# Kernel tuning notes

Measured on AMD Instinct MI355X. Metric: run time of the kernel, lower is better.

## Reference

```python
import jax, jax.numpy as jnp
import numpy as np

N_NODES = 100000
N_EDGES = 1600000
IN_DIM, H1, H2, OUT_DIM = 128, 64, 64, 64


def _glorot(key, shape):
    fan_in, fan_out = shape
    lim = np.sqrt(6.0 / (fan_in + fan_out)).astype(np.float32)
    return jax.random.uniform(key, shape, jnp.float32, -lim, lim)


def setup_inputs() -> dict:
    key = jax.random.key(0)
    ks = jax.random.split(key, 8)
    x = jax.random.normal(ks[0], (N_NODES, IN_DIM), jnp.float32)
    edge_index = jax.random.randint(ks[1], (2, N_EDGES), 0, N_NODES, jnp.int64)
    W1 = _glorot(ks[2], (IN_DIM, H1))
    b1 = jnp.zeros((H1,), jnp.float32)
    W2 = _glorot(ks[3], (H1, H2))
    b2 = jnp.zeros((H2,), jnp.float32)
    Wfc = _glorot(ks[4], (H2, OUT_DIM))
    bfc = jnp.zeros((OUT_DIM,), jnp.float32)
    return {"x": x, "W1": W1, "b1": b1, "W2": W2, "b2": b2,
            "Wfc": Wfc, "bfc": bfc, "edge_index": edge_index}


def _gcn_conv(x, src, dst, dinv, W, b, n_nodes):
    # PyG GCNConv: h = D^{-1/2} (A + I) D^{-1/2} (x W) + b
    h = x @ W                                   # [N, out]
    norm = dinv[src] * dinv[dst]                # [E'] edge weights
    msg = norm[:, None] * h[src]                # gather + scale, [E', out]
    agg = jax.ops.segment_sum(msg, dst, num_segments=n_nodes)
    return agg + b


def reference(x, W1, b1, W2, b2, Wfc, bfc, edge_index):
    n = x.shape[0]
    loop = jnp.arange(n, dtype=edge_index.dtype)
    src = jnp.concatenate([edge_index[0], loop])   # self-loops appended
    dst = jnp.concatenate([edge_index[1], loop])
    deg = jnp.zeros((n,), x.dtype).at[dst].add(1.0)  # degree incl. self-loop
    dinv = jax.lax.rsqrt(deg)

    h = jax.nn.relu(_gcn_conv(x, src, dst, dinv, W1, b1, n))
    h = jax.nn.relu(_gcn_conv(h, src, dst, dinv, W2, b2, n))
    embedding = h
    logits = h @ Wfc + bfc
    return embedding, logits
```

## Files before the change

### kernel.cpp

```cpp
#include <hip/hip_runtime.h>
#include <hip/hip_bf16.h>


constexpr int IN_DIM  = 128;
constexpr int HDIM    = 64;
constexpr int NBLK_A  = 256;
constexpr int BSH     = 8;
constexpr int MAXNB   = 512;

__device__ __forceinline__ float bf2f(unsigned int u) {
    return __uint_as_float(u << 16);
}
__device__ __forceinline__ unsigned short f2bf_bits(float f) {
    __hip_bfloat16 b = __float2bfloat16(f);
    return *(unsigned short*)&b;
}


__global__ void binA_count(const int* __restrict__ dst, int* __restrict__ histg,
                           int E, int NB, int chunk) {
    __shared__ int h[MAXNB];
    for (int i = threadIdx.x; i < NB; i += 256) h[i] = 0;
    __syncthreads();
    int beg = blockIdx.x * chunk;
    int end = min(E, beg + chunk);
    for (int e = beg + threadIdx.x; e < end; e += 256)
        atomicAdd(&h[dst[e] >> BSH], 1);
    __syncthreads();
    for (int i = threadIdx.x; i < NB; i += 256)
        histg[i * NBLK_A + blockIdx.x] = h[i];
}

__global__ void binA_scanblocks(int* __restrict__ histg, int* __restrict__ btot) {
    __shared__ int sm[NBLK_A];
    int tid = threadIdx.x;
    int v = histg[blockIdx.x * NBLK_A + tid];
    sm[tid] = v;
    __syncthreads();
    for (int off = 1; off < NBLK_A; off <<= 1) {
        int t = (tid >= off) ? sm[tid - off] : 0;
        __syncthreads();
        sm[tid] += t;
        __syncthreads();
    }
    histg[blockIdx.x * NBLK_A + tid] = sm[tid] - v;
    if (tid == NBLK_A - 1) btot[blockIdx.x] = sm[tid];
}

__global__ void binA_scanbuckets(const int* __restrict__ btot, int* __restrict__ bucketbase,
                                 int NB) {
    __shared__ int sm[MAXNB];
    int tid = threadIdx.x;
    int v = (tid < NB) ? btot[tid] : 0;
    sm[tid] = v;
    __syncthreads();
    for (int off = 1; off < MAXNB; off <<= 1) {
        int t = (tid >= off) ? sm[tid - off] : 0;
        __syncthreads();
        sm[tid] += t;
        __syncthreads();
    }
    if (tid < NB) bucketbase[tid] = sm[tid] - v;
    if (tid == MAXNB - 1) bucketbase[NB] = sm[tid];
}

__global__ void binA_scatter(const int* __restrict__ src, const int* __restrict__ dst,
                             const int* __restrict__ histg, const int* __restrict__ bucketbase,
                             int* __restrict__ staging, int E, int NB, int chunk) {
    __shared__ int cur[MAXNB];
    for (int i = threadIdx.x; i < NB; i += 256)
        cur[i] = bucketbase[i] + histg[i * NBLK_A + blockIdx.x];
    __syncthreads();
    int beg = blockIdx.x * chunk;
    int end = min(E, beg + chunk);
    for (int e = beg + threadIdx.x; e < end; e += 256) {
        int s = src[e];
        int d = dst[e];
        int pos = atomicAdd(&cur[d >> BSH], 1);
        staging[pos] = (s << BSH) | (d & 255);
    }
}

__global__ void binB_finalize(const int* __restrict__ staging, const int* __restrict__ bucketbase,
                              int* __restrict__ rowptr, int* __restrict__ esrc,
                              float* __restrict__ dinv, int N, int NB) {
    __shared__ int cnt[256], sm[256], cur[256];
    int tid = threadIdx.x;
    int b = blockIdx.x;
    int node0 = b << BSH;
    int nloc = min(256, N - node0);
    int ebeg = bucketbase[b], eend = bucketbase[b + 1];
    cnt[tid] = 0;
    __syncthreads();
    for (int e = ebeg + tid; e < eend; e += 256)
        atomicAdd(&cnt[staging[e] & 255], 1);
    __syncthreads();
    int v = cnt[tid];
    sm[tid] = v;
    __syncthreads();
    for (int off = 1; off < 256; off <<= 1) {
        int t = (tid >= off) ? sm[tid - off] : 0;
        __syncthreads();
        sm[tid] += t;
        __syncthreads();
    }
    int excl = sm[tid] - v;
    cur[tid] = excl;
    __syncthreads();
    if (tid < nloc) {
        rowptr[node0 + tid] = ebeg + excl;
        dinv[node0 + tid] = rsqrtf((float)v + 1.0f);
    }
    if (b == 0 && tid == 0) rowptr[N] = bucketbase[NB];
    for (int e = ebeg + tid; e < eend; e += 256) {
        int p = staging[e];
        int pos = ebeg + atomicAdd(&cur[p & 255], 1);
        esrc[pos] = p >> BSH;
    }
}


template<int K, bool IBF16, bool SCALE, bool BIAS, bool OBF16>
__device__ __forceinline__ void gemm_body(
        const void* __restrict__ Xv, const float* __restrict__ W,
        const float* __restrict__ bias, const float* __restrict__ dinv,
        void* __restrict__ Yv, int n) {
    constexpr int KC = 32;
    constexpr int XSTR = 132;
    __shared__ float Xt[KC * XSTR];
    __shared__ float Ws[KC * 64];
    const int tid = threadIdx.x;
    const int node0 = blockIdx.x * 128;
    const int r0 = (tid >> 4) * 8;
    const int c0 = (tid & 15) * 4;

    float acc[8][4];
#pragma unroll
    for (int a = 0; a < 8; ++a)
#pragma unroll
        for (int b = 0; b < 4; ++b) acc[a][b] = 0.f;

    for (int kc = 0; kc < K; kc += KC) {
        __syncthreads();
#pragma unroll
        for (int i = 0; i < 4; ++i) {
            int s = tid + i * 256;
            int row = s >> 3;
            int kq = s & 7;
            int grow = node0 + row;
            float4 v = make_float4(0.f, 0.f, 0.f, 0.f);
            if (grow < n) {
                if (IBF16) {
                    uint2 u = *(const uint2*)&((const unsigned short*)Xv)[(size_t)grow * K + kc + kq * 4];
                    v.x = bf2f(u.x & 0xffff); v.y = bf2f(u.x >> 16);
                    v.z = bf2f(u.y & 0xffff); v.w = bf2f(u.y >> 16);
                } else {
                    v = *(const float4*)&((const float*)Xv)[(size_t)grow * K + kc + kq * 4];
                }
            }
            Xt[(kq * 4 + 0) * XSTR + row] = v.x;
            Xt[(kq * 4 + 1) * XSTR + row] = v.y;
            Xt[(kq * 4 + 2) * XSTR + row] = v.z;
            Xt[(kq * 4 + 3) * XSTR + row] = v.w;
        }
#pragma unroll
        for (int i = 0; i < 2; ++i) {
            int s = tid + i * 256;
            *(float4*)&Ws[s * 4] = *(const float4*)&W[(size_t)kc * 64 + s * 4];
        }
        __syncthreads();
#pragma unroll
        for (int kk = 0; kk < KC; kk += 4) {
            float4 xa[4][2];
            float4 wv[4];
#pragma unroll
            for (int i = 0; i < 4; ++i) {
                xa[i][0] = *(const float4*)&Xt[(kk + i) * XSTR + r0];
                xa[i][1] = *(const float4*)&Xt[(kk + i) * XSTR + r0 + 4];
                wv[i]    = *(const float4*)&Ws[(kk + i) * 64 + c0];
            }
#pragma unroll
            for (int i = 0; i < 4; ++i) {
                const float* xp = (const float*)&xa[i][0];
                const float* wp = (const float*)&wv[i];
#pragma unroll
                for (int rr = 0; rr < 8; ++rr)
#pragma unroll
                    for (int cc = 0; cc < 4; ++cc)
                        acc[rr][cc] += xp[rr] * wp[cc];
            }
        }
    }
#pragma unroll
    for (int rr = 0; rr < 8; ++rr) {
        int node = node0 + r0 + rr;
        if (node < n) {
            float d = SCALE ? dinv[node] : 1.0f;
            float t[4];
#pragma unroll
            for (int cc = 0; cc < 4; ++cc) {
                float v = acc[rr][cc];
                if (BIAS) v += bias[c0 + cc];
                t[cc] = v * d;
            }
            if (OBF16) {
                __hip_bfloat16 vb[4];
#pragma unroll
                for (int cc = 0; cc < 4; ++cc) vb[cc] = __float2bfloat16(t[cc]);
                *(uint2*)&((__hip_bfloat16*)Yv)[(size_t)node * 64 + c0] = *(uint2*)vb;
            } else {
                *(float4*)&((float*)Yv)[(size_t)node * 64 + c0] = *(float4*)t;
            }
        }
    }
}

__global__ __launch_bounds__(256, 4) void gemm1_kernel(
        const float* X, const float* W, const float* dinv, void* Y, int n) {
    gemm_body<IN_DIM, false, true, false, true>(X, W, nullptr, dinv, Y, n);
}
__global__ __launch_bounds__(256, 4) void gemm2_kernel(
        const void* X, const float* W, const float* dinv, void* Y, int n) {
    gemm_body<HDIM, true, true, false, true>(X, W, nullptr, dinv, Y, n);
}

template<bool OBF16>
__device__ __forceinline__ void agg_body(
        const unsigned short* __restrict__ hp, const int* __restrict__ esrc,
        const int* __restrict__ rowptr, const float* __restrict__ dinv,
        const float* __restrict__ bias, void* __restrict__ out, int n) {
    int node = blockIdx.x * 4 + (threadIdx.x >> 6);
    if (node >= n) return;
    int lane = threadIdx.x & 63;
    int half = lane >> 5;
    int l = lane & 31;
    const unsigned int* hp32 = (const unsigned int*)hp;
    int beg = rowptr[node], end = rowptr[node + 1];

    float ax = 0.f, ay = 0.f;
    {
        unsigned int u = hp32[(size_t)node * 32 + l];
        if (half == 0) { ax = bf2f(u & 0xffff); ay = bf2f(u >> 16); }
    }
    int k = beg;
    for (; k + 16 <= end; k += 16) {
        int s[8];
#pragma unroll
        for (int i = 0; i < 8; ++i) s[i] = esrc[k + 2 * i + half];
        unsigned int u[8];
#pragma unroll
        for (int i = 0; i < 8; ++i) u[i] = hp32[(size_t)s[i] * 32 + l];
        float vx[8], vy[8];
#pragma unroll
        for (int i = 0; i < 8; ++i) { vx[i] = bf2f(u[i] & 0xffff); vy[i] = bf2f(u[i] >> 16); }
        ax += ((vx[0] + vx[1]) + (vx[2] + vx[3])) + ((vx[4] + vx[5]) + (vx[6] + vx[7]));
        ay += ((vy[0] + vy[1]) + (vy[2] + vy[3])) + ((vy[4] + vy[5]) + (vy[6] + vy[7]));
    }
    if (k < end) {
        int s[8];
#pragma unroll
        for (int i = 0; i < 8; ++i) s[i] = esrc[min(k + 2 * i + half, end - 1)];
        unsigned int u[8];
#pragma unroll
        for (int i = 0; i < 8; ++i) u[i] = hp32[(size_t)s[i] * 32 + l];
        float tx = 0.f, ty = 0.f;
#pragma unroll
        for (int i = 0; i < 8; ++i) {
            bool m = (k + 2 * i + half) < end;
            tx += m ? bf2f(u[i] & 0xffff) : 0.f;
            ty += m ? bf2f(u[i] >> 16)    : 0.f;
        }
        ax += tx; ay += ty;
    }
    ax += __shfl_xor(ax, 32, 64);
    ay += __shfl_xor(ay, 32, 64);

    if (half == 0) {
        float d = dinv[node];
        float ox = fmaxf(d * ax + bias[2 * l], 0.f);
        float oy = fmaxf(d * ay + bias[2 * l + 1], 0.f);
        if (OBF16) {
            unsigned int packed = (unsigned int)f2bf_bits(ox) | ((unsigned int)f2bf_bits(oy) << 16);
            ((unsigned int*)out)[(size_t)node * 32 + l] = packed;
        } else {
            float2 o = make_float2(ox, oy);
            ((float2*)out)[(size_t)node * 32 + l] = o;
        }
    }
}

__global__ __launch_bounds__(256) void agg1_kernel(
        const unsigned short* hp, const int* esrc, const int* rowptr,
        const float* dinv, const float* bias, void* out, int n) {
    agg_body<true>(hp, esrc, rowptr, dinv, bias, out, n);
}

__global__ __launch_bounds__(256) void agg2_fc_kernel(
        const unsigned short* __restrict__ hp, const int* __restrict__ esrc,
        const int* __restrict__ rowptr, const float* __restrict__ dinv,
        const float* __restrict__ bias,
        const float* __restrict__ Wfc, const float* __restrict__ bfc,
        float* __restrict__ emb, float* __restrict__ logits, int n) {
    __shared__ float hsm[4][64];
    const int w = threadIdx.x >> 6;
    const int node = blockIdx.x * 4 + w;
    const int lane = threadIdx.x & 63;
    const int half = lane >> 5;
    const int l = lane & 31;
    const bool valid = node < n;

    if (valid) {
        const unsigned int* hp32 = (const unsigned int*)hp;
        int beg = rowptr[node], end = rowptr[node + 1];
        float ax = 0.f, ay = 0.f;
        {
            unsigned int u = hp32[(size_t)node * 32 + l];
            if (half == 0) { ax = bf2f(u & 0xffff); ay = bf2f(u >> 16); }
        }
        int k = beg;
        for (; k + 16 <= end; k += 16) {
            int s[8];
#pragma unroll
            for (int i = 0; i < 8; ++i) s[i] = esrc[k + 2 * i + half];
            unsigned int u[8];
#pragma unroll
            for (int i = 0; i < 8; ++i) u[i] = hp32[(size_t)s[i] * 32 + l];
            float vx[8], vy[8];
#pragma unroll
            for (int i = 0; i < 8; ++i) { vx[i] = bf2f(u[i] & 0xffff); vy[i] = bf2f(u[i] >> 16); }
            ax += ((vx[0] + vx[1]) + (vx[2] + vx[3])) + ((vx[4] + vx[5]) + (vx[6] + vx[7]));
            ay += ((vy[0] + vy[1]) + (vy[2] + vy[3])) + ((vy[4] + vy[5]) + (vy[6] + vy[7]));
        }
        if (k < end) {
            int s[8];
#pragma unroll
            for (int i = 0; i < 8; ++i) s[i] = esrc[min(k + 2 * i + half, end - 1)];
            unsigned int u[8];
#pragma unroll
            for (int i = 0; i < 8; ++i) u[i] = hp32[(size_t)s[i] * 32 + l];
            float tx = 0.f, ty = 0.f;
#pragma unroll
            for (int i = 0; i < 8; ++i) {
                bool m = (k + 2 * i + half) < end;
                tx += m ? bf2f(u[i] & 0xffff) : 0.f;
                ty += m ? bf2f(u[i] >> 16)    : 0.f;
            }
            ax += tx; ay += ty;
        }
        ax += __shfl_xor(ax, 32, 64);
        ay += __shfl_xor(ay, 32, 64);

        if (half == 0) {
            float d = dinv[node];
            float ox = fmaxf(d * ax + bias[2 * l], 0.f);
            float oy = fmaxf(d * ay + bias[2 * l + 1], 0.f);
            ((float2*)emb)[(size_t)node * 32 + l] = make_float2(ox, oy);
            *(float2*)&hsm[w][2 * l] = make_float2(ox, oy);
        }
    } else if (half == 0) {
        *(float2*)&hsm[w][2 * l] = make_float2(0.f, 0.f);
    }
    __syncthreads();

    const int o = lane;
    float acc = bfc[o];
    const float* hrow = hsm[w];
#pragma unroll 16
    for (int f = 0; f < 64; ++f)
        acc += hrow[f] * Wfc[f * 64 + o];
    if (valid) logits[(size_t)node * 64 + o] = acc;
}

extern "C" void kernel_launch(void* const* d_in, const int* in_sizes, int n_in,
                              void* d_out, int out_size, void* d_ws, size_t ws_size,
                              hipStream_t stream) {
    const float* x   = (const float*)d_in[0];
    const float* W1  = (const float*)d_in[1];
    const float* b1  = (const float*)d_in[2];
    const float* W2  = (const float*)d_in[3];
    const float* b2  = (const float*)d_in[4];
    const float* Wfc = (const float*)d_in[5];
    const float* bfc = (const float*)d_in[6];
    const int*  eidx = (const int*)d_in[7];

    const int N = in_sizes[0] / IN_DIM;
    const int E = in_sizes[7] / 2;
    const int* src = eidx;
    const int* dst = eidx + E;

    const int NB    = (N + 255) >> BSH;
    const int chunk = (E + NBLK_A - 1) / NBLK_A;

    int*   rowptr     = (int*)d_ws;
    float* dinv       = (float*)(rowptr + (N + 2));
    int*   histg      = (int*)(dinv + N);
    int*   btot       = histg + (size_t)NB * NBLK_A + (((size_t)NB * NBLK_A) & 1);
    int*   bucketbase = btot + 512;
    int*   esrc       = bucketbase + 512;
    float* bufA       = (float*)(esrc + E + (E & 1));
    float* bufB       = bufA + (size_t)N * HDIM;
    int*   staging    = (int*)bufA;
    unsigned short* hp = (unsigned short*)bufA;
    unsigned short* h1 = (unsigned short*)bufB;

    float* emb    = (float*)d_out;
    float* logits = emb + (size_t)N * HDIM;

    binA_count<<<NBLK_A, 256, 0, stream>>>(dst, histg, E, NB, chunk);
    binA_scanblocks<<<NB, NBLK_A, 0, stream>>>(histg, btot);
    binA_scanbuckets<<<1, MAXNB, 0, stream>>>(btot, bucketbase, NB);
    binA_scatter<<<NBLK_A, 256, 0, stream>>>(src, dst, histg, bucketbase, staging, E, NB, chunk);
    binB_finalize<<<NB, 256, 0, stream>>>(staging, bucketbase, rowptr, esrc, dinv, N, NB);

    const int gBlocks = (N + 127) / 128;
    const int aBlocks = (N + 3) / 4;

    gemm1_kernel<<<gBlocks, 256, 0, stream>>>(x, W1, dinv, hp, N);
    agg1_kernel<<<aBlocks, 256, 0, stream>>>(hp, esrc, rowptr, dinv, b1, h1, N);

    gemm2_kernel<<<gBlocks, 256, 0, stream>>>(h1, W2, dinv, hp, N);

    agg2_fc_kernel<<<aBlocks, 256, 0, stream>>>(hp, esrc, rowptr, dinv, b2,
                                                Wfc, bfc, emb, logits, N);
}
```

Baseline: 328.3 us.

## Split hidden features into two 32-column halves and aggregate each in a separate pass

The GEMMs now write their bf16 outputs as two separate 32-feature planes (64 bytes per node each), and each GCN aggregation runs as two passes, one per half. The aim is to shrink the gathered working set per pass so it fits better in cache (L2/MALL), cutting gather misses on random neighbour reads. Inside each pass a wave now handles 8 edges at a time, each edge read by 8 lanes with 8-byte loads, and the partial sums are combined with shuffles. The cost is reading the edge list and rowptr twice, two extra kernel launches, and a final pass that re-reads the first half of the embedding from global memory before the FC layer.

```diff
diff --git a/kernel.cpp b/kernel.cpp
--- a/kernel.cpp
+++ b/kernel.cpp
@@ -120,11 +120,11 @@
 }
 
 
-template<int K, bool IBF16, bool SCALE, bool BIAS, bool OBF16>
+template<int K, bool IBF16, bool SPLITIN>
 __device__ __forceinline__ void gemm_body(
-        const void* __restrict__ Xv, const float* __restrict__ W,
-        const float* __restrict__ bias, const float* __restrict__ dinv,
-        void* __restrict__ Yv, int n) {
+        const void* __restrict__ XAv, const void* __restrict__ XBv,
+        const float* __restrict__ W, const float* __restrict__ dinv,
+        unsigned short* __restrict__ YA, unsigned short* __restrict__ YB, int n) {
     constexpr int KC = 32;
     constexpr int XSTR = 132;
     __shared__ float Xt[KC * XSTR];
@@ -151,11 +151,16 @@
             float4 v = make_float4(0.f, 0.f, 0.f, 0.f);
             if (grow < n) {
                 if (IBF16) {
-                    uint2 u = *(const uint2*)&((const unsigned short*)Xv)[(size_t)grow * K + kc + kq * 4];
+                    const unsigned short* xb = SPLITIN
+                        ? (const unsigned short*)(kc == 0 ? XAv : XBv)
+                        : (const unsigned short*)XAv;
+                    size_t off = SPLITIN ? ((size_t)grow * 32 + kq * 4)
+                                         : ((size_t)grow * K + kc + kq * 4);
+                    uint2 u = *(const uint2*)&xb[off];
                     v.x = bf2f(u.x & 0xffff); v.y = bf2f(u.x >> 16);
                     v.z = bf2f(u.y & 0xffff); v.w = bf2f(u.y >> 16);
                 } else {
-                    v = *(const float4*)&((const float*)Xv)[(size_t)grow * K + kc + kq * 4];
+                    v = *(const float4*)&((const float*)XAv)[(size_t)grow * K + kc + kq * 4];
                 }
             }
             Xt[(kq * 4 + 0) * XSTR + row] = v.x;
@@ -195,180 +200,127 @@
     for (int rr = 0; rr < 8; ++rr) {
         int node = node0 + r0 + rr;
         if (node < n) {
-            float d = SCALE ? dinv[node] : 1.0f;
-            float t[4];
-#pragma unroll
-            for (int cc = 0; cc < 4; ++cc) {
-                float v = acc[rr][cc];
-                if (BIAS) v += bias[c0 + cc];
-                t[cc] = v * d;
-            }
-            if (OBF16) {
-                __hip_bfloat16 vb[4];
-#pragma unroll
-                for (int cc = 0; cc < 4; ++cc) vb[cc] = __float2bfloat16(t[cc]);
-                *(uint2*)&((__hip_bfloat16*)Yv)[(size_t)node * 64 + c0] = *(uint2*)vb;
-            } else {
-                *(float4*)&((float*)Yv)[(size_t)node * 64 + c0] = *(float4*)t;
-            }
+            float d = dinv[node];
+            __hip_bfloat16 vb[4];
+#pragma unroll
+            for (int cc = 0; cc < 4; ++cc)
+                vb[cc] = __float2bfloat16(acc[rr][cc] * d);
+            unsigned short* Yb = (c0 < 32) ? YA : YB;
+            *(uint2*)&Yb[(size_t)node * 32 + (c0 & 31)] = *(uint2*)vb;
         }
     }
 }
 
 __global__ __launch_bounds__(256, 4) void gemm1_kernel(
-        const float* X, const float* W, const float* dinv, void* Y, int n) {
-    gemm_body<IN_DIM, false, true, false, true>(X, W, nullptr, dinv, Y, n);
+        const float* X, const float* W, const float* dinv,
+        unsigned short* YA, unsigned short* YB, int n) {
+    gemm_body<IN_DIM, false, false>(X, nullptr, W, dinv, YA, YB, n);
 }
 __global__ __launch_bounds__(256, 4) void gemm2_kernel(
-        const void* X, const float* W, const float* dinv, void* Y, int n) {
-    gemm_body<HDIM, true, true, false, true>(X, W, nullptr, dinv, Y, n);
-}
-
-template<bool OBF16>
-__device__ __forceinline__ void agg_body(
-        const unsigned short* __restrict__ hp, const int* __restrict__ esrc,
+        const unsigned short* XA, const unsigned short* XB,
+        const float* W, const float* dinv,
+        unsigned short* YA, unsigned short* YB, int n) {
+    gemm_body<HDIM, true, true>(XA, XB, W, dinv, YA, YB, n);
+}
+
+template<int PASS, bool OBF16, bool FC>
+__global__ __launch_bounds__(256) void agg_pass(
+        const uint2* __restrict__ hpx, const int* __restrict__ esrc,
         const int* __restrict__ rowptr, const float* __restrict__ dinv,
-        const float* __restrict__ bias, void* __restrict__ out, int n) {
-    int node = blockIdx.x * 4 + (threadIdx.x >> 6);
-    if (node >= n) return;
-    int lane = threadIdx.x & 63;
-    int half = lane >> 5;
-    int l = lane & 31;
-    const unsigned int* hp32 = (const unsigned int*)hp;
-    int beg = rowptr[node], end = rowptr[node + 1];
-
-    float ax = 0.f, ay = 0.f;
-    {
-        unsigned int u = hp32[(size_t)node * 32 + l];
-        if (half == 0) { ax = bf2f(u & 0xffff); ay = bf2f(u >> 16); }
-    }
-    int k = beg;
-    for (; k + 16 <= end; k += 16) {
-        int s[8];
-#pragma unroll
-        for (int i = 0; i < 8; ++i) s[i] = esrc[k + 2 * i + half];
-        unsigned int u[8];
-#pragma unroll
-        for (int i = 0; i < 8; ++i) u[i] = hp32[(size_t)s[i] * 32 + l];
-        float vx[8], vy[8];
-#pragma unroll
-        for (int i = 0; i < 8; ++i) { vx[i] = bf2f(u[i] & 0xffff); vy[i] = bf2f(u[i] >> 16); }
-        ax += ((vx[0] + vx[1]) + (vx[2] + vx[3])) + ((vx[4] + vx[5]) + (vx[6] + vx[7]));
-        ay += ((vy[0] + vy[1]) + (vy[2] + vy[3])) + ((vy[4] + vy[5]) + (vy[6] + vy[7]));
-    }
-    if (k < end) {
-        int s[8];
-#pragma unroll
-        for (int i = 0; i < 8; ++i) s[i] = esrc[min(k + 2 * i + half, end - 1)];
-        unsigned int u[8];
-#pragma unroll
-        for (int i = 0; i < 8; ++i) u[i] = hp32[(size_t)s[i] * 32 + l];
-        float tx = 0.f, ty = 0.f;
-#pragma unroll
-        for (int i = 0; i < 8; ++i) {
-            bool m = (k + 2 * i + half) < end;
-            tx += m ? bf2f(u[i] & 0xffff) : 0.f;
-            ty += m ? bf2f(u[i] >> 16)    : 0.f;
-        }
-        ax += tx; ay += ty;
-    }
-    ax += __shfl_xor(ax, 32, 64);
-    ay += __shfl_xor(ay, 32, 64);
-
-    if (half == 0) {
-        float d = dinv[node];
-        float ox = fmaxf(d * ax + bias[2 * l], 0.f);
-        float oy = fmaxf(d * ay + bias[2 * l + 1], 0.f);
-        if (OBF16) {
-            unsigned int packed = (unsigned int)f2bf_bits(ox) | ((unsigned int)f2bf_bits(oy) << 16);
-            ((unsigned int*)out)[(size_t)node * 32 + l] = packed;
-        } else {
-            float2 o = make_float2(ox, oy);
-            ((float2*)out)[(size_t)node * 32 + l] = o;
-        }
-    }
-}
-
-__global__ __launch_bounds__(256) void agg1_kernel(
-        const unsigned short* hp, const int* esrc, const int* rowptr,
-        const float* dinv, const float* bias, void* out, int n) {
-    agg_body<true>(hp, esrc, rowptr, dinv, bias, out, n);
-}
-
-__global__ __launch_bounds__(256) void agg2_fc_kernel(
-        const unsigned short* __restrict__ hp, const int* __restrict__ esrc,
-        const int* __restrict__ rowptr, const float* __restrict__ dinv,
-        const float* __restrict__ bias,
+        const float* __restrict__ bias, void* __restrict__ out,
         const float* __restrict__ Wfc, const float* __restrict__ bfc,
-        float* __restrict__ emb, float* __restrict__ logits, int n) {
+        float* __restrict__ logits, int n) {
     __shared__ float hsm[4][64];
     const int w = threadIdx.x >> 6;
     const int node = blockIdx.x * 4 + w;
     const int lane = threadIdx.x & 63;
-    const int half = lane >> 5;
-    const int l = lane & 31;
+    const int g = lane >> 3;
+    const int j = lane & 7;
     const bool valid = node < n;
 
     if (valid) {
-        const unsigned int* hp32 = (const unsigned int*)hp;
-        int beg = rowptr[node], end = rowptr[node + 1];
-        float ax = 0.f, ay = 0.f;
-        {
-            unsigned int u = hp32[(size_t)node * 32 + l];
-            if (half == 0) { ax = bf2f(u & 0xffff); ay = bf2f(u >> 16); }
+        const int beg = rowptr[node], end = rowptr[node + 1];
+        float a0 = 0.f, a1 = 0.f, a2 = 0.f, a3 = 0.f;
+        if (g == 0) {
+            uint2 u = hpx[(size_t)node * 8 + j];
+            a0 = bf2f(u.x & 0xffff); a1 = bf2f(u.x >> 16);
+            a2 = bf2f(u.y & 0xffff); a3 = bf2f(u.y >> 16);
         }
         int k = beg;
         for (; k + 16 <= end; k += 16) {
-            int s[8];
-#pragma unroll
-            for (int i = 0; i < 8; ++i) s[i] = esrc[k + 2 * i + half];
-            unsigned int u[8];
-#pragma unroll
-            for (int i = 0; i < 8; ++i) u[i] = hp32[(size_t)s[i] * 32 + l];
-            float vx[8], vy[8];
-#pragma unroll
-            for (int i = 0; i < 8; ++i) { vx[i] = bf2f(u[i] & 0xffff); vy[i] = bf2f(u[i] >> 16); }
-            ax += ((vx[0] + vx[1]) + (vx[2] + vx[3])) + ((vx[4] + vx[5]) + (vx[6] + vx[7]));
-            ay += ((vy[0] + vy[1]) + (vy[2] + vy[3])) + ((vy[4] + vy[5]) + (vy[6] + vy[7]));
+            int s0 = esrc[k + g];
+            int s1 = esrc[k + 8 + g];
+            uint2 u0 = hpx[(size_t)s0 * 8 + j];
+            uint2 u1 = hpx[(size_t)s1 * 8 + j];
+            a0 += bf2f(u0.x & 0xffff) + bf2f(u1.x & 0xffff);
+            a1 += bf2f(u0.x >> 16)    + bf2f(u1.x >> 16);
+            a2 += bf2f(u0.y & 0xffff) + bf2f(u1.y & 0xffff);
+            a3 += bf2f(u0.y >> 16)    + bf2f(u1.y >> 16);
         }
         if (k < end) {
-            int s[8];
-#pragma unroll
-            for (int i = 0; i < 8; ++i) s[i] = esrc[min(k + 2 * i + half, end - 1)];
-            unsigned int u[8];
-#pragma unroll
-            for (int i = 0; i < 8; ++i) u[i] = hp32[(size_t)s[i] * 32 + l];
-            float tx = 0.f, ty = 0.f;
-#pragma unroll
-            for (int i = 0; i < 8; ++i) {
-                bool m = (k + 2 * i + half) < end;
-                tx += m ? bf2f(u[i] & 0xffff) : 0.f;
-                ty += m ? bf2f(u[i] >> 16)    : 0.f;
-            }
-            ax += tx; ay += ty;
-        }
-        ax += __shfl_xor(ax, 32, 64);
-        ay += __shfl_xor(ay, 32, 64);
-
-        if (half == 0) {
-            float d = dinv[node];
-            float ox = fmaxf(d * ax + bias[2 * l], 0.f);
-            float oy = fmaxf(d * ay + bias[2 * l + 1], 0.f);
-            ((float2*)emb)[(size_t)node * 32 + l] = make_float2(ox, oy);
-            *(float2*)&hsm[w][2 * l] = make_float2(ox, oy);
-        }
-    } else if (half == 0) {
-        *(float2*)&hsm[w][2 * l] = make_float2(0.f, 0.f);
-    }
-    __syncthreads();
-
-    const int o = lane;
-    float acc = bfc[o];
-    const float* hrow = hsm[w];
+            int e0 = k + g, e1 = k + 8 + g;
+            int s0 = esrc[min(e0, end - 1)];
+            int s1 = esrc[min(e1, end - 1)];
+            uint2 u0 = hpx[(size_t)s0 * 8 + j];
+            uint2 u1 = hpx[(size_t)s1 * 8 + j];
+            if (e0 < end) {
+                a0 += bf2f(u0.x & 0xffff); a1 += bf2f(u0.x >> 16);
+                a2 += bf2f(u0.y & 0xffff); a3 += bf2f(u0.y >> 16);
+            }
+            if (e1 < end) {
+                a0 += bf2f(u1.x & 0xffff); a1 += bf2f(u1.x >> 16);
+                a2 += bf2f(u1.y & 0xffff); a3 += bf2f(u1.y >> 16);
+            }
+        }
+#pragma unroll
+        for (int st = 8; st <= 32; st <<= 1) {
+            a0 += __shfl_xor(a0, st, 64);
+            a1 += __shfl_xor(a1, st, 64);
+            a2 += __shfl_xor(a2, st, 64);
+            a3 += __shfl_xor(a3, st, 64);
+        }
+        const float d = dinv[node];
+        const float v0 = fmaxf(fmaf(d, a0, bias[PASS * 32 + 4 * j + 0]), 0.f);
+        const float v1 = fmaxf(fmaf(d, a1, bias[PASS * 32 + 4 * j + 1]), 0.f);
+        const float v2 = fmaxf(fmaf(d, a2, bias[PASS * 32 + 4 * j + 2]), 0.f);
+        const float v3 = fmaxf(fmaf(d, a3, bias[PASS * 32 + 4 * j + 3]), 0.f);
+
+        if (g == 0) {
+            if (OBF16) {
+                unsigned int p0 = (unsigned int)f2bf_bits(v0) | ((unsigned int)f2bf_bits(v1) << 16);
+                unsigned int p1 = (unsigned int)f2bf_bits(v2) | ((unsigned int)f2bf_bits(v3) << 16);
+                ((uint2*)out)[(size_t)node * 8 + j] = make_uint2(p0, p1);
+            } else {
+                ((float4*)out)[(size_t)node * 16 + PASS * 8 + j] = make_float4(v0, v1, v2, v3);
+            }
+        }
+        if (FC) {
+            if (g == 0) {
+                hsm[w][32 + 4 * j + 0] = v0;
+                hsm[w][32 + 4 * j + 1] = v1;
+                hsm[w][32 + 4 * j + 2] = v2;
+                hsm[w][32 + 4 * j + 3] = v3;
+            } else if (g == 1) {
+                float4 f = ((const float4*)out)[(size_t)node * 16 + j];
+                hsm[w][4 * j + 0] = f.x;
+                hsm[w][4 * j + 1] = f.y;
+                hsm[w][4 * j + 2] = f.z;
+                hsm[w][4 * j + 3] = f.w;
+            }
+        }
+    } else if (FC) {
+        hsm[w][lane] = 0.f;
+    }
+
+    if (FC) {
+        __syncthreads();
+        float acc = bfc[lane];
+        const float* hrow = hsm[w];
 #pragma unroll 16
-    for (int f = 0; f < 64; ++f)
-        acc += hrow[f] * Wfc[f * 64 + o];
-    if (valid) logits[(size_t)node * 64 + o] = acc;
+        for (int f = 0; f < 64; ++f)
+            acc += hrow[f] * Wfc[(size_t)f * 64 + lane];
+        if (valid) logits[(size_t)node * 64 + lane] = acc;
+    }
 }
 
 extern "C" void kernel_launch(void* const* d_in, const int* in_sizes, int n_in,
@@ -391,17 +343,18 @@
     const int NB    = (N + 255) >> BSH;
     const int chunk = (E + NBLK_A - 1) / NBLK_A;
 
-    int*   rowptr     = (int*)d_ws;
-    float* dinv       = (float*)(rowptr + (N + 2));
-    int*   histg      = (int*)(dinv + N);
-    int*   btot       = histg + (size_t)NB * NBLK_A + (((size_t)NB * NBLK_A) & 1);
-    int*   bucketbase = btot + 512;
-    int*   esrc       = bucketbase + 512;
-    float* bufA       = (float*)(esrc + E + (E & 1));
-    float* bufB       = bufA + (size_t)N * HDIM;
-    int*   staging    = (int*)bufA;
-    unsigned short* hp = (unsigned short*)bufA;
-    unsigned short* h1 = (unsigned short*)bufB;
+    int* p = (int*)d_ws;
+    int* rowptr = p;                 p += (size_t)((N + 2 + 3) & ~3);
+    float* dinv = (float*)p;         p += (size_t)((N + 3) & ~3);
+    int* histg = p;                  p += (size_t)((NB * NBLK_A + 3) & ~3);
+    int* btot = p;                   p += 512;
+    int* bucketbase = p;             p += 512;
+    int* esrc = p;                   p += (size_t)((E + 3) & ~3);
+    unsigned short* hpA = (unsigned short*)p;  p += (size_t)N * 16;
+    unsigned short* hpB = (unsigned short*)p;  p += (size_t)N * 16;
+    unsigned short* h1A = (unsigned short*)p;  p += (size_t)N * 16;
+    unsigned short* h1B = (unsigned short*)p;  p += (size_t)N * 16;
+    int* staging = (int*)hpA;
 
     float* emb    = (float*)d_out;
     float* logits = emb + (size_t)N * HDIM;
@@ -415,11 +368,15 @@
     const int gBlocks = (N + 127) / 128;
     const int aBlocks = (N + 3) / 4;
 
-    gemm1_kernel<<<gBlocks, 256, 0, stream>>>(x, W1, dinv, hp, N);
-    agg1_kernel<<<aBlocks, 256, 0, stream>>>(hp, esrc, rowptr, dinv, b1, h1, N);
-
-    gemm2_kernel<<<gBlocks, 256, 0, stream>>>(h1, W2, dinv, hp, N);
-
-    agg2_fc_kernel<<<aBlocks, 256, 0, stream>>>(hp, esrc, rowptr, dinv, b2,
-                                                Wfc, bfc, emb, logits, N);
-}
+    gemm1_kernel<<<gBlocks, 256, 0, stream>>>(x, W1, dinv, hpA, hpB, N);
+    agg_pass<0, true, false><<<aBlocks, 256, 0, stream>>>(
+        (const uint2*)hpA, esrc, rowptr, dinv, b1, h1A, nullptr, nullptr, nullptr, N);
+    agg_pass<1, true, false><<<aBlocks, 256, 0, stream>>>(
+        (const uint2*)hpB, esrc, rowptr, dinv, b1, h1B, nullptr, nullptr, nullptr, N);
+
+    gemm2_kernel<<<gBlocks, 256, 0, stream>>>(h1A, h1B, W2, dinv, hpA, hpB, N);
+    agg_pass<0, false, false><<<aBlocks, 256, 0, stream>>>(
+        (const uint2*)hpA, esrc, rowptr, dinv, b2, emb, nullptr, nullptr, nullptr, N);
+    agg_pass<1, false, true><<<aBlocks, 256, 0, stream>>>(
+        (const uint2*)hpB, esrc, rowptr, dinv, b2, emb, Wfc, bfc, logits, N);
+}
```

Result: slower. 395.1 us (+20.3%).

## Pad CSR rows to multiples of eight and aggregate with 8 lanes per node

Applied to the files above, without the earlier changes.

Each node's edge list is padded to a multiple of 8 with a dummy source N whose feature row is zeroed, so the aggregation loop needs no tail masking. Each node is now handled by 8 lanes doing 16-byte gathers instead of a full wavefront doing 4-byte gathers, which raises memory-level parallelism and cuts idle lanes on low-degree nodes. The fused agg2+FC kernel is split into a plain aggregation and a separate FC GEMM pass reading the embedding back. Costs are extra padded edges, a larger workspace, and one more kernel launch plus an extra read of the embedding.

```diff
diff --git a/kernel.cpp b/kernel.cpp
--- a/kernel.cpp
+++ b/kernel.cpp
@@ -7,6 +7,7 @@
 constexpr int NBLK_A  = 256;
 constexpr int BSH     = 8;
 constexpr int MAXNB   = 512;
+constexpr int PADSLK  = 1792;
 
 __device__ __forceinline__ float bf2f(unsigned int u) {
     return __uint_as_float(u << 16);
@@ -82,21 +83,24 @@
 }
 
 __global__ void binB_finalize(const int* __restrict__ staging, const int* __restrict__ bucketbase,
-                              int* __restrict__ rowptr, int* __restrict__ esrc,
-                              float* __restrict__ dinv, int N, int NB) {
+                              int2* __restrict__ rows, int* __restrict__ esrc,
+                              float* __restrict__ dinv, unsigned int* __restrict__ hp_rowN,
+                              int N, int NB) {
     __shared__ int cnt[256], sm[256], cur[256];
     int tid = threadIdx.x;
     int b = blockIdx.x;
     int node0 = b << BSH;
     int nloc = min(256, N - node0);
     int ebeg = bucketbase[b], eend = bucketbase[b + 1];
+    int ebegP = ebeg + b * PADSLK;
     cnt[tid] = 0;
     __syncthreads();
     for (int e = ebeg + tid; e < eend; e += 256)
         atomicAdd(&cnt[staging[e] & 255], 1);
     __syncthreads();
     int v = cnt[tid];
-    sm[tid] = v;
+    int pv = (v + 7) & ~7;
+    sm[tid] = pv;
     __syncthreads();
     for (int off = 1; off < 256; off <<= 1) {
         int t = (tid >= off) ? sm[tid - off] : 0;
@@ -104,17 +108,19 @@
         sm[tid] += t;
         __syncthreads();
     }
-    int excl = sm[tid] - v;
+    int excl = sm[tid] - pv;
     cur[tid] = excl;
     __syncthreads();
     if (tid < nloc) {
-        rowptr[node0 + tid] = ebeg + excl;
+        rows[node0 + tid] = make_int2(ebegP + excl, ebegP + excl + pv);
         dinv[node0 + tid] = rsqrtf((float)v + 1.0f);
-    }
-    if (b == 0 && tid == 0) rowptr[N] = bucketbase[NB];
+        for (int q = v; q < pv; ++q)
+            esrc[ebegP + excl + q] = N;
+    }
+    if (b == 0 && tid < 32) hp_rowN[tid] = 0u;
     for (int e = ebeg + tid; e < eend; e += 256) {
         int p = staging[e];
-        int pos = ebeg + atomicAdd(&cur[p & 255], 1);
+        int pos = ebegP + atomicAdd(&cur[p & 255], 1);
         esrc[pos] = p >> BSH;
     }
 }
@@ -223,152 +229,64 @@
         const void* X, const float* W, const float* dinv, void* Y, int n) {
     gemm_body<HDIM, true, true, false, true>(X, W, nullptr, dinv, Y, n);
 }
+__global__ __launch_bounds__(256, 4) void fc_kernel(
+        const float* X, const float* W, const float* bias, void* Y, int n) {
+    gemm_body<HDIM, false, false, true, false>(X, W, bias, nullptr, Y, n);
+}
 
 template<bool OBF16>
-__device__ __forceinline__ void agg_body(
-        const unsigned short* __restrict__ hp, const int* __restrict__ esrc,
-        const int* __restrict__ rowptr, const float* __restrict__ dinv,
+__global__ __launch_bounds__(256) void agg_kernel(
+        const uint4* __restrict__ hp4, const int* __restrict__ esrc,
+        const int2* __restrict__ rows, const float* __restrict__ dinv,
         const float* __restrict__ bias, void* __restrict__ out, int n) {
-    int node = blockIdx.x * 4 + (threadIdx.x >> 6);
+    const int lane = threadIdx.x & 63;
+    const int j = lane & 7;
+    const int node = blockIdx.x * 32 + (threadIdx.x >> 6) * 8 + (lane >> 3);
     if (node >= n) return;
-    int lane = threadIdx.x & 63;
-    int half = lane >> 5;
-    int l = lane & 31;
-    const unsigned int* hp32 = (const unsigned int*)hp;
-    int beg = rowptr[node], end = rowptr[node + 1];
-
-    float ax = 0.f, ay = 0.f;
+    const int2 be = rows[node];
+
+    float acc[8];
     {
-        unsigned int u = hp32[(size_t)node * 32 + l];
-        if (half == 0) { ax = bf2f(u & 0xffff); ay = bf2f(u >> 16); }
-    }
-    int k = beg;
-    for (; k + 16 <= end; k += 16) {
+        uint4 u = hp4[(size_t)node * 8 + j];
+        acc[0] = bf2f(u.x & 0xffff); acc[1] = bf2f(u.x >> 16);
+        acc[2] = bf2f(u.y & 0xffff); acc[3] = bf2f(u.y >> 16);
+        acc[4] = bf2f(u.z & 0xffff); acc[5] = bf2f(u.z >> 16);
+        acc[6] = bf2f(u.w & 0xffff); acc[7] = bf2f(u.w >> 16);
+    }
+    for (int k = be.x; k < be.y; k += 8) {
         int s[8];
 #pragma unroll
-        for (int i = 0; i < 8; ++i) s[i] = esrc[k + 2 * i + half];
-        unsigned int u[8];
-#pragma unroll
-        for (int i = 0; i < 8; ++i) u[i] = hp32[(size_t)s[i] * 32 + l];
-        float vx[8], vy[8];
-#pragma unroll
-        for (int i = 0; i < 8; ++i) { vx[i] = bf2f(u[i] & 0xffff); vy[i] = bf2f(u[i] >> 16); }
-        ax += ((vx[0] + vx[1]) + (vx[2] + vx[3])) + ((vx[4] + vx[5]) + (vx[6] + vx[7]));
-        ay += ((vy[0] + vy[1]) + (vy[2] + vy[3])) + ((vy[4] + vy[5]) + (vy[6] + vy[7]));
-    }
-    if (k < end) {
-        int s[8];
-#pragma unroll
-        for (int i = 0; i < 8; ++i) s[i] = esrc[min(k + 2 * i + half, end - 1)];
-        unsigned int u[8];
-#pragma unroll
-        for (int i = 0; i < 8; ++i) u[i] = hp32[(size_t)s[i] * 32 + l];
-        float tx = 0.f, ty = 0.f;
+        for (int i = 0; i < 8; ++i)
+            s[i] = __builtin_nontemporal_load(&esrc[k + i]);
+        uint4 u[8];
+#pragma unroll
+        for (int i = 0; i < 8; ++i)
+            u[i] = hp4[(size_t)s[i] * 8 + j];
 #pragma unroll
         for (int i = 0; i < 8; ++i) {
-            bool m = (k + 2 * i + half) < end;
-            tx += m ? bf2f(u[i] & 0xffff) : 0.f;
-            ty += m ? bf2f(u[i] >> 16)    : 0.f;
-        }
-        ax += tx; ay += ty;
-    }
-    ax += __shfl_xor(ax, 32, 64);
-    ay += __shfl_xor(ay, 32, 64);
-
-    if (half == 0) {
-        float d = dinv[node];
-        float ox = fmaxf(d * ax + bias[2 * l], 0.f);
-        float oy = fmaxf(d * ay + bias[2 * l + 1], 0.f);
-        if (OBF16) {
-            unsigned int packed = (unsigned int)f2bf_bits(ox) | ((unsigned int)f2bf_bits(oy) << 16);
-            ((unsigned int*)out)[(size_t)node * 32 + l] = packed;
-        } else {
-            float2 o = make_float2(ox, oy);
-            ((float2*)out)[(size_t)node * 32 + l] = o;
-        }
-    }
-}
-
-__global__ __launch_bounds__(256) void agg1_kernel(
-        const unsigned short* hp, const int* esrc, const int* rowptr,
-        const float* dinv, const float* bias, void* out, int n) {
-    agg_body<true>(hp, esrc, rowptr, dinv, bias, out, n);
-}
-
-__global__ __launch_bounds__(256) void agg2_fc_kernel(
-        const unsigned short* __restrict__ hp, const int* __restrict__ esrc,
-        const int* __restrict__ rowptr, const float* __restrict__ dinv,
-        const float* __restrict__ bias,
-        const float* __restrict__ Wfc, const float* __restrict__ bfc,
-        float* __restrict__ emb, float* __restrict__ logits, int n) {
-    __shared__ float hsm[4][64];
-    const int w = threadIdx.x >> 6;
-    const int node = blockIdx.x * 4 + w;
-    const int lane = threadIdx.x & 63;
-    const int half = lane >> 5;
-    const int l = lane & 31;
-    const bool valid = node < n;
-
-    if (valid) {
-        const unsigned int* hp32 = (const unsigned int*)hp;
-        int beg = rowptr[node], end = rowptr[node + 1];
-        float ax = 0.f, ay = 0.f;
-        {
-            unsigned int u = hp32[(size_t)node * 32 + l];
-            if (half == 0) { ax = bf2f(u & 0xffff); ay = bf2f(u >> 16); }
-        }
-        int k = beg;
-        for (; k + 16 <= end; k += 16) {
-            int s[8];
-#pragma unroll
-            for (int i = 0; i < 8; ++i) s[i] = esrc[k + 2 * i + half];
-            unsigned int u[8];
-#pragma unroll
-            for (int i = 0; i < 8; ++i) u[i] = hp32[(size_t)s[i] * 32 + l];
-            float vx[8], vy[8];
-#pragma unroll
-            for (int i = 0; i < 8; ++i) { vx[i] = bf2f(u[i] & 0xffff); vy[i] = bf2f(u[i] >> 16); }
-            ax += ((vx[0] + vx[1]) + (vx[2] + vx[3])) + ((vx[4] + vx[5]) + (vx[6] + vx[7]));
-            ay += ((vy[0] + vy[1]) + (vy[2] + vy[3])) + ((vy[4] + vy[5]) + (vy[6] + vy[7]));
-        }
-        if (k < end) {
-            int s[8];
-#pragma unroll
-            for (int i = 0; i < 8; ++i) s[i] = esrc[min(k + 2 * i + half, end - 1)];
-            unsigned int u[8];
-#pragma unroll
-            for (int i = 0; i < 8; ++i) u[i] = hp32[(size_t)s[i] * 32 + l];
-            float tx = 0.f, ty = 0.f;
-#pragma unroll
-            for (int i = 0; i < 8; ++i) {
-                bool m = (k + 2 * i + half) < end;
-                tx += m ? bf2f(u[i] & 0xffff) : 0.f;
-                ty += m ? bf2f(u[i] >> 16)    : 0.f;
-            }
-            ax += tx; ay += ty;
-        }
-        ax += __shfl_xor(ax, 32, 64);
-        ay += __shfl_xor(ay, 32, 64);
-
-        if (half == 0) {
-            float d = dinv[node];
-            float ox = fmaxf(d * ax + bias[2 * l], 0.f);
-            float oy = fmaxf(d * ay + bias[2 * l + 1], 0.f);
-            ((float2*)emb)[(size_t)node * 32 + l] = make_float2(ox, oy);
-            *(float2*)&hsm[w][2 * l] = make_float2(ox, oy);
-        }
-    } else if (half == 0) {
-        *(float2*)&hsm[w][2 * l] = make_float2(0.f, 0.f);
-    }
-    __syncthreads();
-
-    const int o = lane;
-    float acc = bfc[o];
-    const float* hrow = hsm[w];
-#pragma unroll 16
-    for (int f = 0; f < 64; ++f)
-        acc += hrow[f] * Wfc[f * 64 + o];
-    if (valid) logits[(size_t)node * 64 + o] = acc;
+            acc[0] += bf2f(u[i].x & 0xffff); acc[1] += bf2f(u[i].x >> 16);
+            acc[2] += bf2f(u[i].y & 0xffff); acc[3] += bf2f(u[i].y >> 16);
+            acc[4] += bf2f(u[i].z & 0xffff); acc[5] += bf2f(u[i].z >> 16);
+            acc[6] += bf2f(u[i].w & 0xffff); acc[7] += bf2f(u[i].w >> 16);
+        }
+    }
+    const float d = dinv[node];
+    float o[8];
+#pragma unroll
+    for (int t = 0; t < 8; ++t)
+        o[t] = fmaxf(fmaf(d, acc[t], bias[8 * j + t]), 0.f);
+
+    if (OBF16) {
+        uint4 pk;
+        pk.x = (unsigned)f2bf_bits(o[0]) | ((unsigned)f2bf_bits(o[1]) << 16);
+        pk.y = (unsigned)f2bf_bits(o[2]) | ((unsigned)f2bf_bits(o[3]) << 16);
+        pk.z = (unsigned)f2bf_bits(o[4]) | ((unsigned)f2bf_bits(o[5]) << 16);
+        pk.w = (unsigned)f2bf_bits(o[6]) | ((unsigned)f2bf_bits(o[7]) << 16);
+        ((uint4*)out)[(size_t)node * 8 + j] = pk;
+    } else {
+        ((float4*)out)[(size_t)node * 16 + 2 * j]     = make_float4(o[0], o[1], o[2], o[3]);
+        ((float4*)out)[(size_t)node * 16 + 2 * j + 1] = make_float4(o[4], o[5], o[6], o[7]);
+    }
 }
 
 extern "C" void kernel_launch(void* const* d_in, const int* in_sizes, int n_in,
@@ -390,18 +308,19 @@
 
     const int NB    = (N + 255) >> BSH;
     const int chunk = (E + NBLK_A - 1) / NBLK_A;
-
-    int*   rowptr     = (int*)d_ws;
-    float* dinv       = (float*)(rowptr + (N + 2));
-    int*   histg      = (int*)(dinv + N);
-    int*   btot       = histg + (size_t)NB * NBLK_A + (((size_t)NB * NBLK_A) & 1);
-    int*   bucketbase = btot + 512;
-    int*   esrc       = bucketbase + 512;
-    float* bufA       = (float*)(esrc + E + (E & 1));
-    float* bufB       = bufA + (size_t)N * HDIM;
-    int*   staging    = (int*)bufA;
-    unsigned short* hp = (unsigned short*)bufA;
-    unsigned short* h1 = (unsigned short*)bufB;
+    const int EP    = E + NB * PADSLK;
+
+    int* p = (int*)d_ws;
+    int2* rows = (int2*)p;           p += (size_t)2 * N + 2;
+    float* dinv = (float*)p;         p += (size_t)((N + 3) & ~3);
+    int* histg = p;                  p += (size_t)((NB * NBLK_A + 3) & ~3);
+    int* btot = p;                   p += 512;
+    int* bucketbase = p;             p += 512;
+    int* esrc = p;                   p += (size_t)((EP + 3) & ~3);
+    unsigned short* hp = (unsigned short*)p;   p += (size_t)(N + 1) * 32;
+    unsigned short* h1 = (unsigned short*)p;   p += (size_t)N * 32;
+    int* staging = (int*)hp;
+    unsigned int* hp_rowN = (unsigned int*)(hp + (size_t)N * 64);
 
     float* emb    = (float*)d_out;
     float* logits = emb + (size_t)N * HDIM;
@@ -410,16 +329,18 @@
     binA_scanblocks<<<NB, NBLK_A, 0, stream>>>(histg, btot);
     binA_scanbuckets<<<1, MAXNB, 0, stream>>>(btot, bucketbase, NB);
     binA_scatter<<<NBLK_A, 256, 0, stream>>>(src, dst, histg, bucketbase, staging, E, NB, chunk);
-    binB_finalize<<<NB, 256, 0, stream>>>(staging, bucketbase, rowptr, esrc, dinv, N, NB);
+    binB_finalize<<<NB, 256, 0, stream>>>(staging, bucketbase, rows, esrc, dinv, hp_rowN, N, NB);
 
     const int gBlocks = (N + 127) / 128;
-    const int aBlocks = (N + 3) / 4;
+    const int aBlocks = (N + 31) / 32;
 
     gemm1_kernel<<<gBlocks, 256, 0, stream>>>(x, W1, dinv, hp, N);
-    agg1_kernel<<<aBlocks, 256, 0, stream>>>(hp, esrc, rowptr, dinv, b1, h1, N);
+    agg_kernel<true><<<aBlocks, 256, 0, stream>>>(
+        (const uint4*)hp, esrc, rows, dinv, b1, h1, N);
 
     gemm2_kernel<<<gBlocks, 256, 0, stream>>>(h1, W2, dinv, hp, N);
-
-    agg2_fc_kernel<<<aBlocks, 256, 0, stream>>>(hp, esrc, rowptr, dinv, b2,
-                                                Wfc, bfc, emb, logits, N);
-}
+    agg_kernel<false><<<aBlocks, 256, 0, stream>>>(
+        (const uint4*)hp, esrc, rows, dinv, b2, emb, N);
+
+    fc_kernel<<<gBlocks, 256, 0, stream>>>(emb, Wfc, bfc, logits, N);
+}
```

After: 315.4 us. 1.04x faster.
